# Optimization experiments

Hardware: AMD Instinct MI355X
Metric: run time of the kernel (lower is better)

The kernel has to match this reference:

```python
import jax, jax.numpy as jnp
import numpy as np

ROW, COL, KSIZE = 7, 7, 5   # unfold_row, unfold_column, kernel_size
EPS = 1e-5


def _unfold(x, row, col):
    # non-overlapping nn.Unfold(kernel=(row,col), stride=(row,col)) -> [B*L, C, row, col]
    B, C, H, W = x.shape
    nr, nc = H // row, W // col
    return x.reshape(B, C, nr, row, nc, col).transpose(0, 2, 4, 1, 3, 5).reshape(B * nr * nc, C, row, col)


def _fold(x, B, H, W):
    BL, C, row, col = x.shape
    nr, nc = H // row, W // col
    return x.reshape(B, nr, nc, C, row, col).transpose(0, 3, 1, 4, 2, 5).reshape(B, C, H, W)


def _bilinear_shift(img, yq, xq):
    # out[n,i,j] = img[n, yq[n,i], xq[n,j]] with bilinear interp, zeros outside
    # (matches F.grid_sample(align_corners=True, padding_mode='zeros') for pure translations)
    N, H, W = img.shape
    y0 = jnp.floor(yq); x0 = jnp.floor(xq)
    fy = yq - y0; fx = xq - x0
    y0 = y0.astype(jnp.int32); x0 = x0.astype(jnp.int32)
    out = jnp.zeros_like(img)
    for dy, wy in ((0, 1.0 - fy), (1, fy)):
        yi = y0 + dy
        vy = wy * ((yi >= 0) & (yi < H)).astype(img.dtype)                              # [N,H]
        rows = jnp.take_along_axis(img, jnp.clip(yi, 0, H - 1)[:, :, None], axis=1)     # [N,H,W]
        for dx, wx in ((0, 1.0 - fx), (1, fx)):
            xi = x0 + dx
            vx = wx * ((xi >= 0) & (xi < W)).astype(img.dtype)                          # [N,W]
            vals = jnp.take_along_axis(rows, jnp.clip(xi, 0, W - 1)[:, None, :], axis=2)
            out = out + vy[:, :, None] * vx[:, None, :] * vals
    return out


def setup_inputs():
    key = jax.random.key(0)
    k1, k2, k3 = jax.random.split(key, 3)
    feat = jax.random.normal(k1, (16, 8, 126, 126), jnp.float32)
    # encoder logits are class probabilities over the 100 Gaussian prototypes
    logits = jax.nn.softmax(jax.random.normal(k2, (16, 100, 126, 126), jnp.float32), axis=1)
    s = jnp.linspace(0.2, 3.0, 10)
    sx, sy = jnp.meshgrid(s, s, indexing='ij')            # matches torch.meshgrid init
    sigma_x = sx.reshape(-1)
    sigma_y = sy.reshape(-1)
    opacity = jax.nn.sigmoid(jnp.ones((100,), jnp.float32))
    rho = jax.random.uniform(k3, (100,), jnp.float32, -0.5, 0.5)
    return {"feat": feat, "logits": logits, "sigma_x": sigma_x,
            "sigma_y": sigma_y, "opacity": opacity, "rho": rho}


def reference(feat, logits, sigma_x, sigma_y, opacity, rho):
    B, C, H, W = feat.shape
    # H, W are multiples of ROW/COL so the bicubic resize to the ceil-multiple size is identity
    uf = _unfold(feat, ROW, COL)        # [BL, C, 7, 7]
    ul = _unfold(logits, ROW, COL)      # [BL, 100, 7, 7]
    BL = uf.shape[0]
    N = ROW * COL                        # 49 points per patch
    # weighted_gaussian_parameters: contract over class dim, then mean over batch(=B*L)
    lg = ul.transpose(0, 2, 3, 1)        # [BL, 7, 7, 100]
    wsx = (lg * sigma_x).sum(-1).reshape(BL, N).mean(0)   # [N]
    wsy = (lg * sigma_y).sum(-1).reshape(BL, N).mean(0)
    wop = (lg * opacity).sum(-1).reshape(BL, N).mean(0)
    wrho = (lg * rho).sum(-1).reshape(BL, N).mean(0)
    # 2x2 covariance per point; analytic inverse / det
    a = wsx * wsx + EPS
    d = wsy * wsy + EPS
    b = wrho * wsx * wsy
    det = a * d - b * b                                    # [N], > 0
    ax = jnp.linspace(-5.0, 5.0, KSIZE)
    gx, gy = jnp.meshgrid(ax, ax, indexing='ij')           # [K,K]
    z = -0.5 * (d[:, None, None] * gx**2 - 2.0 * b[:, None, None] * gx * gy
                + a[:, None, None] * gy**2) / det[:, None, None]
    kern = jnp.exp(z) / (2.0 * jnp.pi * jnp.sqrt(det)[:, None, None])
    kern = kern / kern.max(axis=(-2, -1), keepdims=True)   # [N,K,K], max-normalized
    # pad kernel up to the patch raster size
    ph, pw = ROW - KSIZE, COL - KSIZE
    kern = jnp.pad(kern, ((0, 0), (ph // 2, ph - ph // 2), (pw // 2, pw - pw // 2)))
    # translate kernel p to its point location (affine_grid/grid_sample semantics)
    ii, jj = jnp.meshgrid(jnp.arange(ROW), jnp.arange(COL), indexing='ij')
    yp = ii.reshape(-1).astype(kern.dtype)                 # p = y*COL + x (generate_meshgrid order)
    xp = jj.reshape(-1).astype(kern.dtype)
    tx = (1.0 - 2.0 * xp / ROW) * (COL - 1) / 2.0          # divisor ROW mirrors original (ROW==COL)
    ty = (1.0 - 2.0 * yp / COL) * (ROW - 1) / 2.0
    xq = jnp.arange(COL, dtype=kern.dtype)[None, :] + tx[:, None]   # [N,COL]
    yq = jnp.arange(ROW, dtype=kern.dtype)[None, :] + ty[:, None]   # [N,ROW]
    kt = _bilinear_shift(kern, yq, xq)                     # [N,7,7]
    # colors at each point are the patch pixel values (fetching_features_from_tensor)
    colors = uf.reshape(BL, C, N).transpose(0, 2, 1)       # [BL,N,C]
    # splat: sum_p color[bl,p,c] * opacity_w[p] * kernel_p(i,j)  (fused, avoids [BL,N,C,7,7])
    out = jnp.einsum('lpc,p,pij->lcij', colors, wop, kt)
    return _fold(out, B, H, W)
```

## Files before the change

kernel.cpp:

```cpp
#include <hip/hip_runtime.h>

#define W 126
#define NPIX 15876
#define NB 16
#define NCH 8
#define NCLS 100

#define GR 3
#define CC 10
#define NYCH 10
#define NWAVES (NYCH * NB * 7 * 6)
#define NBLK_A (NWAVES / 4)

#define WS_ACC_OFF 0
#define WS_MT_OFF 256
#define WS_PART_OFF 4096

__global__ __launch_bounds__(256) void ga_reduce(
    const float* __restrict__ logits,
    const float* __restrict__ sx, const float* __restrict__ sy,
    const float* __restrict__ op, const float* __restrict__ rho,
    float* __restrict__ part) {
  __shared__ float s_data[4][64][8];
  __shared__ float s_bin[196];
  __shared__ int   s_m[4];
  const int t    = threadIdx.x;
  const int w    = t >> 6;
  const int lane = t & 63;

  for (int i = t; i < 196; i += 256) s_bin[i] = 0.f;

  const int wid = blockIdx.x * 4 + w;
  const int cy  = wid / 672;
  int rem = wid - cy * 672;
  const int b   = rem / 42;
  rem -= b * 42;
  const int m   = rem / 6;
  const int yg  = rem - m * 6;
  if (lane == 0) s_m[w] = m;

  float a[4][2];
#pragma unroll
  for (int k = 0; k < 4; ++k) { a[k][0] = 0.f; a[k][1] = 0.f; }

  if (lane < 63) {
    const int c0 = cy * CC;
#pragma unroll
    for (int r = 0; r < GR; ++r) {
      const int y = m + 7 * (yg * GR + r);
      const float2* rowb = reinterpret_cast<const float2*>(
          logits + ((size_t)(b * NCLS) * W + y) * W) + lane;
      float2 v[CC];
#pragma unroll
      for (int cc = 0; cc < CC; ++cc)
        v[cc] = rowb[(size_t)(c0 + cc) * (NPIX / 2)];
#pragma unroll
      for (int cc = 0; cc < CC; ++cc) {
        const int c = c0 + cc;
        const float p0 = sx[c], p1 = sy[c], p2 = op[c], p3 = rho[c];
        a[0][0] += v[cc].x * p0; a[0][1] += v[cc].y * p0;
        a[1][0] += v[cc].x * p1; a[1][1] += v[cc].y * p1;
        a[2][0] += v[cc].x * p2; a[2][1] += v[cc].y * p2;
        a[3][0] += v[cc].x * p3; a[3][1] += v[cc].y * p3;
      }
    }
  }

#pragma unroll
  for (int k = 0; k < 4; ++k) {
    s_data[w][lane][k * 2]     = a[k][0];
    s_data[w][lane][k * 2 + 1] = a[k][1];
  }
  __syncthreads();

  if (t < 112) {
    const int ww = t / 28;
    const int k  = (t % 28) / 7;
    const int n  = t % 7;
    float s = 0.f;
#pragma unroll
    for (int j = 0; j < 18; ++j) {
      const int p = n + 7 * j;
      s += s_data[ww][p >> 1][k * 2 + (p & 1)];
    }
    atomicAdd(&s_bin[k * 49 + s_m[ww] * 7 + n], s);
  }
  __syncthreads();

  float* my = part + (size_t)blockIdx.x * 196;
  for (int i = t; i < 196; i += 256) my[i] = s_bin[i];
}

__global__ __launch_bounds__(256) void ga_final(const float* __restrict__ part,
                                                float* __restrict__ acc) {
  __shared__ float4 red[256];
  const int h = blockIdx.x;
  const int t = threadIdx.x;
  float4 s = make_float4(0.f, 0.f, 0.f, 0.f);
  for (int j = t; j < NBLK_A; j += 256) {
    const float4 v =
        *reinterpret_cast<const float4*>(part + (size_t)j * 196 + h * 4);
    s.x += v.x; s.y += v.y; s.z += v.z; s.w += v.w;
  }
  red[t] = s;
  __syncthreads();
#pragma unroll
  for (int off = 128; off; off >>= 1) {
    if (t < off) {
      red[t].x += red[t + off].x; red[t].y += red[t + off].y;
      red[t].z += red[t + off].z; red[t].w += red[t + off].w;
    }
    __syncthreads();
  }
  if (t == 0) *reinterpret_cast<float4*>(acc + h * 4) = red[0];
}

__global__ __launch_bounds__(64) void gb_build(const float* __restrict__ acc,
                                               float* __restrict__ MT) {
  __shared__ float s_kern[49][49];
  const int p = threadIdx.x;
  for (int i = p; i < 49; i += 64) {
    MT[i * 52 + 49] = 0.f;
    MT[i * 52 + 50] = 0.f;
    MT[i * 52 + 51] = 0.f;
  }
  if (p < 49) {
    const float inv = 1.0f / 5184.0f;
    const float wsx = acc[p]        * inv;
    const float wsy = acc[49 + p]   * inv;
    const float wop = acc[98 + p]   * inv;
    const float wrh = acc[147 + p]  * inv;
    const float av = wsx * wsx + 1e-5f;
    const float dv = wsy * wsy + 1e-5f;
    const float bv = wrh * wsx * wsy;
    const float det = av * dv - bv * bv;
    const float norm = 1.0f / (6.283185307179586f * sqrtf(det));
    float tmp[5][5];
    float mx = 0.f;
#pragma unroll
    for (int i = 0; i < 5; ++i) {
      const float gx = -5.0f + 2.5f * (float)i;
#pragma unroll
      for (int j = 0; j < 5; ++j) {
        const float gy = -5.0f + 2.5f * (float)j;
        const float z = -0.5f * (dv*gx*gx - 2.0f*bv*gx*gy + av*gy*gy) / det;
        const float v = expf(z) * norm;
        tmp[i][j] = v;
        mx = fmaxf(mx, v);
      }
    }
    const float rmx = 1.0f / mx;
#pragma unroll
    for (int i = 0; i < 49; ++i) s_kern[p][i] = 0.f;
#pragma unroll
    for (int i = 0; i < 5; ++i)
#pragma unroll
      for (int j = 0; j < 5; ++j)
        s_kern[p][(i + 1) * 7 + (j + 1)] = tmp[i][j] * rmx;

    const int yp = p / 7, xp = p % 7;
    const float tx = (1.0f - (2.0f * (float)xp) / 7.0f) * 3.0f;
    const float ty = (1.0f - (2.0f * (float)yp) / 7.0f) * 3.0f;
    for (int i = 0; i < 7; ++i) {
      const float yq  = (float)i + ty;
      const float y0f = floorf(yq);
      const float fy  = yq - y0f;
      const int   y0  = (int)y0f;
      for (int j = 0; j < 7; ++j) {
        const float xq  = (float)j + tx;
        const float x0f = floorf(xq);
        const float fx  = xq - x0f;
        const int   x0  = (int)x0f;
        float v = 0.f;
        for (int dy = 0; dy < 2; ++dy) {
          const int yi = y0 + dy;
          if (yi < 0 || yi > 6) continue;
          const float wy = dy ? fy : (1.0f - fy);
          for (int dx = 0; dx < 2; ++dx) {
            const int xi = x0 + dx;
            if (xi < 0 || xi > 6) continue;
            const float wx = dx ? fx : (1.0f - fx);
            v += wy * wx * s_kern[p][yi * 7 + xi];
          }
        }
        MT[(i * 7 + j) * 52 + p] = wop * v;
      }
    }
  }
}

__global__ __launch_bounds__(256) void gc_splat(
    const float* __restrict__ feat, const float* __restrict__ MT,
    float* __restrict__ out) {
  __shared__ __align__(16) float s_mt[49 * 52];
  __shared__ __align__(16) float s_fp[18 * 52];
  const int t = threadIdx.x;
  for (int i = t; i < 49 * 52; i += 256) s_mt[i] = MT[i];
  const int blk   = blockIdx.x;
  const int plane = blk / 18;
  const int pr    = blk - plane * 18;
  const float* src = feat + (size_t)plane * NPIX + (size_t)pr * 7 * W;
  for (int i = t; i < 882; i += 256) {
    const int py = i / W;
    const int xx = i - py * W;
    const int pc = xx / 7;
    const int px = xx - pc * 7;
    s_fp[pc * 52 + py * 7 + px] = src[i];
  }
  __syncthreads();
  float* dst = out + (size_t)plane * NPIX + (size_t)pr * 7 * W;
  for (int i = t; i < 882; i += 256) {
    const int yy = i / W;
    const int xx = i - yy * W;
    const int pc = xx / 7;
    const int q  = yy * 7 + (xx - pc * 7);
    const float4* mv = reinterpret_cast<const float4*>(s_mt + q * 52);
    const float4* fv = reinterpret_cast<const float4*>(s_fp + pc * 52);
    float s = 0.f;
#pragma unroll
    for (int r = 0; r < 12; ++r) {
      const float4 mm = mv[r];
      const float4 ff = fv[r];
      s += ff.x * mm.x + ff.y * mm.y + ff.z * mm.z + ff.w * mm.w;
    }
    s += s_fp[pc * 52 + 48] * s_mt[q * 52 + 48];
    dst[i] = s;
  }
}

extern "C" void kernel_launch(void* const* d_in, const int* in_sizes, int n_in,
                              void* d_out, int out_size, void* d_ws, size_t ws_size,
                              hipStream_t stream) {
  const float* feat   = (const float*)d_in[0];
  const float* logits = (const float*)d_in[1];
  const float* sx     = (const float*)d_in[2];
  const float* sy     = (const float*)d_in[3];
  const float* op     = (const float*)d_in[4];
  const float* rho    = (const float*)d_in[5];
  float* outp = (float*)d_out;
  float* ws   = (float*)d_ws;
  float* acc  = ws + WS_ACC_OFF;
  float* MT   = ws + WS_MT_OFF;
  float* part = ws + WS_PART_OFF;

  ga_reduce<<<NBLK_A, 256, 0, stream>>>(logits, sx, sy, op, rho, part);
  ga_final<<<49, 256, 0, stream>>>(part, acc);
  gb_build<<<1, 64, 0, stream>>>(acc, MT);
  gc_splat<<<NB * NCH * 18, 256, 0, stream>>>(feat, MT, outp);
}
```

Baseline: 61.59 us.

## Register-tile splat over 3 patches x 7 columns and batch logits row loads

The splat kernel now has each block handle three patch rows with 128 threads. Each thread computes a 3x7 output tile in registers, so feature and matrix float4 reads from LDS are reused across outputs. Padding lanes are zeroed to allow 13 full float4 steps. The reduce kernel issues all 30 row loads up front to raise memory-level parallelism, and its LDS scratch is padded to 9 to avoid bank conflicts. The risks are higher register pressure and uncoalesced strided 21-element output stores per thread.

```diff
diff --git a/kernel.cpp b/kernel.cpp
--- a/kernel.cpp
+++ b/kernel.cpp
@@ -21,7 +21,7 @@
     const float* __restrict__ sx, const float* __restrict__ sy,
     const float* __restrict__ op, const float* __restrict__ rho,
     float* __restrict__ part) {
-  __shared__ float s_data[4][64][8];
+  __shared__ float s_data[4][64][9];
   __shared__ float s_bin[196];
   __shared__ int   s_m[4];
   const int t    = threadIdx.x;
@@ -45,25 +45,38 @@
 
   if (lane < 63) {
     const int c0 = cy * CC;
-#pragma unroll
-    for (int r = 0; r < GR; ++r) {
-      const int y = m + 7 * (yg * GR + r);
-      const float2* rowb = reinterpret_cast<const float2*>(
-          logits + ((size_t)(b * NCLS) * W + y) * W) + lane;
-      float2 v[CC];
-#pragma unroll
-      for (int cc = 0; cc < CC; ++cc)
-        v[cc] = rowb[(size_t)(c0 + cc) * (NPIX / 2)];
-#pragma unroll
-      for (int cc = 0; cc < CC; ++cc) {
-        const int c = c0 + cc;
-        const float p0 = sx[c], p1 = sy[c], p2 = op[c], p3 = rho[c];
-        a[0][0] += v[cc].x * p0; a[0][1] += v[cc].y * p0;
-        a[1][0] += v[cc].x * p1; a[1][1] += v[cc].y * p1;
-        a[2][0] += v[cc].x * p2; a[2][1] += v[cc].y * p2;
-        a[3][0] += v[cc].x * p3; a[3][1] += v[cc].y * p3;
-      }
-    }
+    const float* img = logits + (size_t)b * NCLS * NPIX + (size_t)c0 * NPIX;
+    const int y0 = m + 7 * (yg * GR);
+    const float2* r0 =
+        reinterpret_cast<const float2*>(img + (size_t)y0 * W) + lane;
+    const float2* r1 =
+        reinterpret_cast<const float2*>(img + (size_t)(y0 + 7) * W) + lane;
+    const float2* r2 =
+        reinterpret_cast<const float2*>(img + (size_t)(y0 + 14) * W) + lane;
+
+    float2 v0[CC], v1[CC], v2[CC];
+#pragma unroll
+    for (int cc = 0; cc < CC; ++cc) v0[cc] = r0[(size_t)cc * (NPIX / 2)];
+#pragma unroll
+    for (int cc = 0; cc < CC; ++cc) v1[cc] = r1[(size_t)cc * (NPIX / 2)];
+#pragma unroll
+    for (int cc = 0; cc < CC; ++cc) v2[cc] = r2[(size_t)cc * (NPIX / 2)];
+
+#define FMA_ROW(V)                                                   \
+    _Pragma("unroll")                                                \
+    for (int cc = 0; cc < CC; ++cc) {                                \
+      const int c = c0 + cc;                                         \
+      const float p0 = sx[c], p1 = sy[c];                            \
+      const float p2 = op[c], p3 = rho[c];                           \
+      a[0][0] += V[cc].x * p0; a[0][1] += V[cc].y * p0;              \
+      a[1][0] += V[cc].x * p1; a[1][1] += V[cc].y * p1;              \
+      a[2][0] += V[cc].x * p2; a[2][1] += V[cc].y * p2;              \
+      a[3][0] += V[cc].x * p3; a[3][1] += V[cc].y * p3;              \
+    }
+    FMA_ROW(v0)
+    FMA_ROW(v1)
+    FMA_ROW(v2)
+#undef FMA_ROW
   }
 
 #pragma unroll
@@ -189,42 +202,72 @@
   }
 }
 
-__global__ __launch_bounds__(256) void gc_splat(
+__global__ __launch_bounds__(128) void gc_splat(
     const float* __restrict__ feat, const float* __restrict__ MT,
     float* __restrict__ out) {
   __shared__ __align__(16) float s_mt[49 * 52];
-  __shared__ __align__(16) float s_fp[18 * 52];
+  __shared__ __align__(16) float s_fp[3 * 18 * 52];
   const int t = threadIdx.x;
-  for (int i = t; i < 49 * 52; i += 256) s_mt[i] = MT[i];
-  const int blk   = blockIdx.x;
-  const int plane = blk / 18;
-  const int pr    = blk - plane * 18;
-  const float* src = feat + (size_t)plane * NPIX + (size_t)pr * 7 * W;
-  for (int i = t; i < 882; i += 256) {
-    const int py = i / W;
-    const int xx = i - py * W;
-    const int pc = xx / 7;
-    const int px = xx - pc * 7;
-    s_fp[pc * 52 + py * 7 + px] = src[i];
-  }
-  __syncthreads();
-  float* dst = out + (size_t)plane * NPIX + (size_t)pr * 7 * W;
-  for (int i = t; i < 882; i += 256) {
-    const int yy = i / W;
-    const int xx = i - yy * W;
-    const int pc = xx / 7;
-    const int q  = yy * 7 + (xx - pc * 7);
-    const float4* mv = reinterpret_cast<const float4*>(s_mt + q * 52);
-    const float4* fv = reinterpret_cast<const float4*>(s_fp + pc * 52);
-    float s = 0.f;
-#pragma unroll
-    for (int r = 0; r < 12; ++r) {
-      const float4 mm = mv[r];
-      const float4 ff = fv[r];
-      s += ff.x * mm.x + ff.y * mm.y + ff.z * mm.z + ff.w * mm.w;
-    }
-    s += s_fp[pc * 52 + 48] * s_mt[q * 52 + 48];
-    dst[i] = s;
+  {
+    const float4* s4 = reinterpret_cast<const float4*>(MT);
+    float4* d4 = reinterpret_cast<float4*>(s_mt);
+    for (int i = t; i < (49 * 52) / 4; i += 128) d4[i] = s4[i];
+  }
+  for (int i = t; i < 3 * 18; i += 128) {
+    s_fp[i * 52 + 49] = 0.f;
+    s_fp[i * 52 + 50] = 0.f;
+    s_fp[i * 52 + 51] = 0.f;
+  }
+  const int plane = blockIdx.x / 6;
+  const int sg    = blockIdx.x - plane * 6;
+  const float* src = feat + (size_t)plane * NPIX + (size_t)sg * (21 * W);
+  for (int i = t; i < 21 * W; i += 128) {
+    const int y  = i / W;
+    const int x  = i - y * W;
+    const int s  = y / 7, py = y - s * 7;
+    const int pc = x / 7, px = x - pc * 7;
+    s_fp[(s * 18 + pc) * 52 + py * 7 + px] = src[i];
+  }
+  __syncthreads();
+
+  if (t < 126) {
+    const int s  = t / 42;
+    const int rm = t - s * 42;
+    const int g  = rm / 7;
+    const int yy = rm - g * 7;
+    const float* mrow = s_mt + (yy * 7) * 52;
+    const float* frow = s_fp + (s * 18 + 3 * g) * 52;
+
+    float acc[3][7];
+#pragma unroll
+    for (int j = 0; j < 3; ++j)
+#pragma unroll
+      for (int xx = 0; xx < 7; ++xx) acc[j][xx] = 0.f;
+
+#pragma unroll
+    for (int r = 0; r < 13; ++r) {
+      float4 fv[3];
+#pragma unroll
+      for (int j = 0; j < 3; ++j)
+        fv[j] = *reinterpret_cast<const float4*>(frow + j * 52 + 4 * r);
+#pragma unroll
+      for (int xx = 0; xx < 7; ++xx) {
+        const float4 mv =
+            *reinterpret_cast<const float4*>(mrow + xx * 52 + 4 * r);
+#pragma unroll
+        for (int j = 0; j < 3; ++j)
+          acc[j][xx] +=
+              fv[j].x * mv.x + fv[j].y * mv.y + fv[j].z * mv.z + fv[j].w * mv.w;
+      }
+    }
+
+    float* dst = out + (size_t)plane * NPIX +
+                 (size_t)((3 * sg + s) * 7 + yy) * W + 21 * g;
+#pragma unroll
+    for (int j = 0; j < 3; ++j)
+#pragma unroll
+      for (int xx = 0; xx < 7; ++xx)
+        dst[j * 7 + xx] = acc[j][xx];
   }
 }
 
@@ -246,5 +289,5 @@
   ga_reduce<<<NBLK_A, 256, 0, stream>>>(logits, sx, sy, op, rho, part);
   ga_final<<<49, 256, 0, stream>>>(part, acc);
   gb_build<<<1, 64, 0, stream>>>(acc, MT);
-  gc_splat<<<NB * NCH * 18, 256, 0, stream>>>(feat, MT, outp);
-}
+  gc_splat<<<NB * NCH * 6, 128, 0, stream>>>(feat, MT, outp);
+}
```

Result: slower. 69.74 us (+13.2%).

## Load logits as float4 over row pairs in ga_reduce

Applied to the files above, without the earlier changes.

Each wave in the reduction kernel now covers two consecutive image rows (252 floats) and reads them with float4 loads, replacing the earlier pattern of float2 loads across three strided rows. Work is split into 63 row-pairs per batch instead of 7x6 groups, and the shared-memory binning is reworked so that each value maps to its row-within-patch bin. The intent is wider, more contiguous global loads on the dominant logits read. In exchange each thread holds more registers and the block uses a larger padded shared array.

```diff
diff --git a/kernel.cpp b/kernel.cpp
--- a/kernel.cpp
+++ b/kernel.cpp
@@ -6,11 +6,11 @@
 #define NCH 8
 #define NCLS 100
 
-#define GR 3
 #define CC 10
 #define NYCH 10
-#define NWAVES (NYCH * NB * 7 * 6)
-#define NBLK_A (NWAVES / 4)
+#define NPAIR 63
+#define NWID (NYCH * NB * NPAIR)
+#define NBLK_A (NWID / 4)
 
 #define WS_ACC_OFF 0
 #define WS_MT_OFF 256
@@ -21,7 +21,7 @@
     const float* __restrict__ sx, const float* __restrict__ sy,
     const float* __restrict__ op, const float* __restrict__ rho,
     float* __restrict__ part) {
-  __shared__ float s_data[4][64][8];
+  __shared__ float s_data[4][64][17];
   __shared__ float s_bin[196];
   __shared__ int   s_m[4];
   const int t    = threadIdx.x;
@@ -30,60 +30,65 @@
 
   for (int i = t; i < 196; i += 256) s_bin[i] = 0.f;
 
-  const int wid = blockIdx.x * 4 + w;
-  const int cy  = wid / 672;
-  int rem = wid - cy * 672;
-  const int b   = rem / 42;
-  rem -= b * 42;
-  const int m   = rem / 6;
-  const int yg  = rem - m * 6;
+  const int wid  = blockIdx.x * 4 + w;
+  const int cy   = wid / (NB * NPAIR);
+  int rem = wid - cy * (NB * NPAIR);
+  const int b    = rem / NPAIR;
+  const int pair = rem - b * NPAIR;
+  const int m    = (2 * pair) % 7;
   if (lane == 0) s_m[w] = m;
 
-  float a[4][2];
-#pragma unroll
-  for (int k = 0; k < 4; ++k) { a[k][0] = 0.f; a[k][1] = 0.f; }
+  float a[4][4];
+#pragma unroll
+  for (int k = 0; k < 4; ++k)
+#pragma unroll
+    for (int e = 0; e < 4; ++e) a[k][e] = 0.f;
 
   if (lane < 63) {
     const int c0 = cy * CC;
-#pragma unroll
-    for (int r = 0; r < GR; ++r) {
-      const int y = m + 7 * (yg * GR + r);
-      const float2* rowb = reinterpret_cast<const float2*>(
-          logits + ((size_t)(b * NCLS) * W + y) * W) + lane;
-      float2 v[CC];
-#pragma unroll
-      for (int cc = 0; cc < CC; ++cc)
-        v[cc] = rowb[(size_t)(c0 + cc) * (NPIX / 2)];
-#pragma unroll
-      for (int cc = 0; cc < CC; ++cc) {
-        const int c = c0 + cc;
-        const float p0 = sx[c], p1 = sy[c], p2 = op[c], p3 = rho[c];
-        a[0][0] += v[cc].x * p0; a[0][1] += v[cc].y * p0;
-        a[1][0] += v[cc].x * p1; a[1][1] += v[cc].y * p1;
-        a[2][0] += v[cc].x * p2; a[2][1] += v[cc].y * p2;
-        a[3][0] += v[cc].x * p3; a[3][1] += v[cc].y * p3;
-      }
+    const float4* base = reinterpret_cast<const float4*>(
+        logits + ((size_t)b * NCLS + c0) * NPIX + (size_t)pair * 252) + lane;
+
+    float4 v[CC];
+#pragma unroll
+    for (int cc = 0; cc < CC; ++cc) v[cc] = base[(size_t)cc * (NPIX / 4)];
+
+#pragma unroll
+    for (int cc = 0; cc < CC; ++cc) {
+      const int c = c0 + cc;
+      const float4 vv = v[cc];
+      const float p0 = sx[c], p1 = sy[c], p2 = op[c], p3 = rho[c];
+      a[0][0] += vv.x * p0; a[0][1] += vv.y * p0; a[0][2] += vv.z * p0; a[0][3] += vv.w * p0;
+      a[1][0] += vv.x * p1; a[1][1] += vv.y * p1; a[1][2] += vv.z * p1; a[1][3] += vv.w * p1;
+      a[2][0] += vv.x * p2; a[2][1] += vv.y * p2; a[2][2] += vv.z * p2; a[2][3] += vv.w * p2;
+      a[3][0] += vv.x * p3; a[3][1] += vv.y * p3; a[3][2] += vv.z * p3; a[3][3] += vv.w * p3;
     }
   }
 
 #pragma unroll
   for (int k = 0; k < 4; ++k) {
-    s_data[w][lane][k * 2]     = a[k][0];
-    s_data[w][lane][k * 2 + 1] = a[k][1];
-  }
-  __syncthreads();
-
-  if (t < 112) {
-    const int ww = t / 28;
-    const int k  = (t % 28) / 7;
-    const int n  = t % 7;
+    s_data[w][lane][k * 4 + 0] = a[k][0];
+    s_data[w][lane][k * 4 + 1] = a[k][1];
+    s_data[w][lane][k * 4 + 2] = a[k][2];
+    s_data[w][lane][k * 4 + 3] = a[k][3];
+  }
+  __syncthreads();
+
+  if (t < 224) {
+    const int ww  = t / 56;
+    const int r56 = t - ww * 56;
+    const int k   = r56 / 14;
+    const int rr  = r56 - k * 14;
+    const int rs  = rr / 7;
+    const int n   = rr - rs * 7;
     float s = 0.f;
 #pragma unroll
     for (int j = 0; j < 18; ++j) {
-      const int p = n + 7 * j;
-      s += s_data[ww][p >> 1][k * 2 + (p & 1)];
-    }
-    atomicAdd(&s_bin[k * 49 + s_m[ww] * 7 + n], s);
+      const int f = rs * 126 + n + 7 * j;
+      s += s_data[ww][f >> 2][k * 4 + (f & 3)];
+    }
+    const int mrow = (s_m[ww] + rs) % 7;
+    atomicAdd(&s_bin[k * 49 + mrow * 7 + n], s);
   }
   __syncthreads();
 
```

Result: no change. 62.47 us (+1.4%).
